# Performance work log

Measured on AMD Instinct MI355X. Metric: run time of the kernel, lower is better.

The kernel has to match this reference:

```python
import jax, jax.numpy as jnp
import numpy as np

ROPE_BASE = 10000.0
NEG_INF = jnp.finfo(jnp.float32).min


def _rope(x, pos):
    # x: [B, L, H, D], pos: [L] absolute positions. Rotate-half RoPE.
    D = x.shape[-1]
    half = D // 2
    inv_freq = 1.0 / (ROPE_BASE ** (jnp.arange(half, dtype=jnp.float32) / half))
    ang = pos.astype(jnp.float32)[:, None] * inv_freq  # [L, half]
    cos = jnp.cos(ang)[None, :, None, :]
    sin = jnp.sin(ang)[None, :, None, :]
    x1, x2 = x[..., :half], x[..., half:]
    return jnp.concatenate([x1 * cos - x2 * sin, x1 * sin + x2 * cos], axis=-1)


def setup_inputs() -> dict:
    key = jax.random.key(0)
    kq, kk, kv = jax.random.split(key, 3)
    B, L, H, Dh = 4, 4096, 16, 64
    return {
        "q": jax.random.normal(kq, (B, L, H, Dh), dtype=jnp.float32),
        "k": jax.random.normal(kk, (B, L, H, Dh), dtype=jnp.float32),
        "v": jax.random.normal(kv, (B, L, H, Dh), dtype=jnp.float32),
        "chunk_size": 1024,
        "start_index": 0,
    }


def reference(q, k, v, chunk_size, start_index):
    B, L, H, Dh = q.shape
    Dv = v.shape[-1]
    C = chunk_size
    assert L % C == 0  # chosen shapes avoid padding; original pads otherwise
    n = L // C
    # Per-chunk RoPE with offset start_index + chunk_offset equals
    # full-sequence RoPE at absolute positions start_index + arange(L).
    pos = start_index + jnp.arange(L)
    q_rot = _rope(q.astype(jnp.float32), pos)
    k_rot = _rope(k.astype(jnp.float32), pos)
    qc = q_rot.reshape(B, n, C, H, Dh)
    kc = k_rot.reshape(B, n, C, H, Dh)
    vc = v.astype(jnp.float32).reshape(B, n, C, H, Dv)
    # Unscaled (scale=1.0) block-diagonal causal attention.
    scores = jnp.einsum("bnqhd,bnkhd->bnhqk", qc, kc)
    causal = jnp.tril(jnp.ones((C, C), dtype=jnp.bool_))
    scores = jnp.where(causal, scores, NEG_INF)
    attn = jax.nn.softmax(scores, axis=-1)
    attn = jnp.where(jnp.isnan(attn), 0.0, attn)
    out = jnp.einsum("bnhqk,bnkhd->bnqhd", attn, vc)
    return out.reshape(B, L, H, Dv).astype(q.dtype)
```

## Files before the change

### kernel.cpp

```cpp
#include <hip/hip_runtime.h>

typedef _Float16 f16x8 __attribute__((ext_vector_type(8)));
typedef _Float16 f16x4 __attribute__((ext_vector_type(4)));
typedef float    f32x4 __attribute__((ext_vector_type(4)));
typedef float    f32x16 __attribute__((ext_vector_type(16)));

#define B_N    4
#define L_TOT  4096
#define H_N    16
#define DH     64
#define HALF_D 32
#define QT     64
#define KT     64
#define LDSP   72

#define LOG2_BASE 13.287712379549449f
#define LOG2E     1.4426950408889634f

#define TAB_BYTES  ((size_t)L_TOT * 64 * sizeof(float))
#define IMG_BYTES  ((size_t)B_N * H_N * 64 * 8192)

__global__ void rope_table_kernel(const int* __restrict__ sidx, float* __restrict__ tab) {
    int idx = blockIdx.x * 256 + (int)threadIdx.x;
    if (idx >= L_TOT * HALF_D) return;
    int l = idx >> 5;
    int j = idx & 31;
    float invf = exp2f(-(float)j * (LOG2_BASE / (float)HALF_D));
    float ang = (float)(sidx[0] + l) * invf;
    float s, c;
    sincosf(ang, &s, &c);
    tab[l * 64 + j] = c;
    tab[l * 64 + HALF_D + j] = s;
}

__global__ __launch_bounds__(256)
void prep_kernel(const float* __restrict__ k, const float* __restrict__ v,
                 const float* __restrict__ tab,
                 unsigned char* __restrict__ kimg, unsigned char* __restrict__ vimg)
{
    __shared__ float Vs[64][65];
    int bid = (int)blockIdx.x;
    int t = (int)threadIdx.x;

    if (bid < 4096) {
        int task = bid * 256 + t;
        int c = task & 3;
        int rowid = task >> 2;
        int l = rowid & (L_TOT - 1);
        int bh = rowid >> 12;
        int b = bh >> 4, h = bh & 15;
        int d0 = c * 8;
        const float* src = k + (((size_t)b * L_TOT + l) * H_N + h) * (size_t)DH;
        f32x4 x1a = *(const f32x4*)(src + d0);
        f32x4 x1b = *(const f32x4*)(src + d0 + 4);
        f32x4 x2a = *(const f32x4*)(src + d0 + HALF_D);
        f32x4 x2b = *(const f32x4*)(src + d0 + HALF_D + 4);
        const float* tr = tab + (size_t)l * 64 + d0;
        f32x4 ca = *(const f32x4*)(tr);
        f32x4 cb = *(const f32x4*)(tr + 4);
        f32x4 sa = *(const f32x4*)(tr + HALF_D);
        f32x4 sb = *(const f32x4*)(tr + HALF_D + 4);
        f16x8 olo, ohi;
#pragma unroll
        for (int j = 0; j < 4; ++j) {
            olo[j]     = (_Float16)(x1a[j] * ca[j] - x2a[j] * sa[j]);
            olo[j + 4] = (_Float16)(x1b[j] * cb[j] - x2b[j] * sb[j]);
            ohi[j]     = (_Float16)(x1a[j] * sa[j] + x2a[j] * ca[j]);
            ohi[j + 4] = (_Float16)(x1b[j] * sb[j] + x2b[j] * cb[j]);
        }
        size_t tile = (size_t)bh * 64 + (l >> 6);
        unsigned char* dst = kimg + tile * 8192 + (size_t)(l & 63) * 128;
        int sw = (c ^ (l & 7)) << 4;
        *(f16x8*)(dst + sw)        = olo;
        *(f16x8*)(dst + (sw ^ 64)) = ohi;
    } else {
        int vb = bid - 4096;
        int tile = vb & 63;
        int h = (vb >> 6) & 15;
        int b = vb >> 10;
        int kbase = tile * 64;
        int row = t >> 2, cb = t & 3;
        const float* src = v + (((size_t)b * L_TOT + kbase + row) * H_N + h) * (size_t)DH + cb * 16;
        f32x4 a0 = *(const f32x4*)(src);
        f32x4 a1 = *(const f32x4*)(src + 4);
        f32x4 a2 = *(const f32x4*)(src + 8);
        f32x4 a3 = *(const f32x4*)(src + 12);
#pragma unroll
        for (int j = 0; j < 4; ++j) {
            Vs[row][cb * 16 + j]      = a0[j];
            Vs[row][cb * 16 + 4 + j]  = a1[j];
            Vs[row][cb * 16 + 8 + j]  = a2[j];
            Vs[row][cb * 16 + 12 + j] = a3[j];
        }
        __syncthreads();
        size_t tbase = ((size_t)(b * 16 + h) * 64 + tile) * 8192;
#pragma unroll
        for (int e = 0; e < 2; ++e) {
            int task = e * 256 + t;
            int dv = task >> 3, c = task & 7;
            f16x8 o;
#pragma unroll
            for (int j = 0; j < 8; ++j) o[j] = (_Float16)Vs[8 * c + j][dv];
            *(f16x8*)(vimg + tbase + (size_t)dv * 128 + ((c ^ (dv & 7)) << 4)) = o;
        }
    }
}

__device__ __forceinline__ void gl_lds16(const void* g, void* lds) {
    __builtin_amdgcn_global_load_lds(
        (const __attribute__((address_space(1))) unsigned int*)g,
        (__attribute__((address_space(3))) unsigned int*)lds, 16, 0, 0);
}

__device__ __forceinline__ unsigned pku(float a, float b) {
    return __builtin_bit_cast(unsigned, __builtin_amdgcn_cvt_pkrtz(a, b));
}

__global__ __launch_bounds__(128, 2)
void attn_main_kernel(const float* __restrict__ q, const int* __restrict__ csz,
                      const float* __restrict__ tab,
                      const unsigned char* __restrict__ kimg,
                      const unsigned char* __restrict__ vimg,
                      float* __restrict__ out) {
    __shared__ __align__(16) unsigned char smem[32768];

    const int tid  = (int)threadIdx.x;
    const int lane = tid & 63;
    const int w    = tid >> 6;
    const int qi   = lane & 31;
    const int h    = lane >> 5;
    const int e7   = lane & 7;

    const int bid0  = (int)blockIdx.x;
    const int wg    = (bid0 & 7) * 512 + (bid0 >> 3);
    const int qx    = wg & 63;
    const int hh    = (wg >> 6) & 15;
    const int b     = wg >> 10;

    const int C   = csz[0];
    const int tpc = C >> 6;
    const int qtile = qx ^ ((tpc - 1) & 63);
    const int kb0 = (qtile / tpc) * tpc;

    const int qg = qtile * QT + 32 * w + qi;
    const int qloc = 32 * w + qi;

    const float* qs = q + (((size_t)b * L_TOT + qg) * H_N + hh) * (size_t)DH;
    const int d0 = 8 * h;
    f32x4 xa0 = *(const f32x4*)(qs + d0);       f32x4 xa1 = *(const f32x4*)(qs + d0 + 4);
    f32x4 xb0 = *(const f32x4*)(qs + d0 + 16);  f32x4 xb1 = *(const f32x4*)(qs + d0 + 20);
    f32x4 xc0 = *(const f32x4*)(qs + d0 + 32);  f32x4 xc1 = *(const f32x4*)(qs + d0 + 36);
    f32x4 xd0 = *(const f32x4*)(qs + d0 + 48);  f32x4 xd1 = *(const f32x4*)(qs + d0 + 52);
    const float* tr = tab + (size_t)qg * 64;
    f32x4 ca0 = *(const f32x4*)(tr + d0);       f32x4 ca1 = *(const f32x4*)(tr + d0 + 4);
    f32x4 cb0 = *(const f32x4*)(tr + d0 + 16);  f32x4 cb1 = *(const f32x4*)(tr + d0 + 20);
    f32x4 sa0 = *(const f32x4*)(tr + 32 + d0);      f32x4 sa1 = *(const f32x4*)(tr + 32 + d0 + 4);
    f32x4 sb0 = *(const f32x4*)(tr + 32 + d0 + 16); f32x4 sb1 = *(const f32x4*)(tr + 32 + d0 + 20);
    f16x8 qf0, qf1, qf2, qf3;
#pragma unroll
    for (int j = 0; j < 4; ++j) {
        qf0[j]     = (_Float16)((xa0[j] * ca0[j] - xc0[j] * sa0[j]) * LOG2E);
        qf0[j + 4] = (_Float16)((xa1[j] * ca1[j] - xc1[j] * sa1[j]) * LOG2E);
        qf1[j]     = (_Float16)((xb0[j] * cb0[j] - xd0[j] * sb0[j]) * LOG2E);
        qf1[j + 4] = (_Float16)((xb1[j] * cb1[j] - xd1[j] * sb1[j]) * LOG2E);
        qf2[j]     = (_Float16)((xa0[j] * sa0[j] + xc0[j] * ca0[j]) * LOG2E);
        qf2[j + 4] = (_Float16)((xa1[j] * sa1[j] + xc1[j] * ca1[j]) * LOG2E);
        qf3[j]     = (_Float16)((xb0[j] * sb0[j] + xd0[j] * cb0[j]) * LOG2E);
        qf3[j + 4] = (_Float16)((xb1[j] * sb1[j] + xd1[j] * cb1[j]) * LOG2E);
    }

    const unsigned char* ksrc = kimg + (size_t)(b * 16 + hh) * 64 * 8192;
    const unsigned char* vsrc = vimg + (size_t)(b * 16 + hh) * 64 * 8192;

    const int rbase = qi * 128;

    f32x16 acc0 = {}, acc1 = {};
    float m = -3e38f, l = 0.f;

    {
        const unsigned char* gk = ksrc + (size_t)kb0 * 8192;
        const unsigned char* gv = vsrc + (size_t)kb0 * 8192;
#pragma unroll
        for (int e = 0; e < 4; ++e) {
            gl_lds16(gk + tid * 16 + e * 2048, smem + tid * 16 + e * 2048);
            gl_lds16(gv + tid * 16 + e * 2048, smem + 16384 + tid * 16 + e * 2048);
        }
    }

    int pb = 0;
    for (int kb = kb0; kb <= qtile; ++kb) {
        __syncthreads();

        const char* Kb = (const char*)(smem + pb * 8192);
        const char* Vb = (const char*)(smem + 16384 + pb * 8192);
        if (kb < qtile) {
            const unsigned char* nk = ksrc + (size_t)(kb + 1) * 8192;
            const unsigned char* nv = vsrc + (size_t)(kb + 1) * 8192;
            unsigned char* lk = smem + (pb ^ 1) * 8192;
            unsigned char* lv = smem + 16384 + (pb ^ 1) * 8192;
#pragma unroll
            for (int e = 0; e < 4; ++e) {
                gl_lds16(nk + tid * 16 + e * 2048, lk + tid * 16 + e * 2048);
                gl_lds16(nv + tid * 16 + e * 2048, lv + tid * 16 + e * 2048);
            }
        }

        f32x16 sc0 = {}, sc1 = {};
        __builtin_amdgcn_s_setprio(1);
#pragma unroll
        for (int s = 0; s < 4; ++s) {
            f16x8 kf = *(const f16x8*)(Kb + rbase + (((h + 2 * s) ^ e7) << 4));
            const f16x8 qv = (s == 0) ? qf0 : (s == 1) ? qf1 : (s == 2) ? qf2 : qf3;
            sc0 = __builtin_amdgcn_mfma_f32_32x32x16_f16(kf, qv, sc0, 0, 0, 0);
        }
#pragma unroll
        for (int s = 0; s < 4; ++s) {
            f16x8 kf = *(const f16x8*)(Kb + 4096 + rbase + (((h + 2 * s) ^ e7) << 4));
            const f16x8 qv = (s == 0) ? qf0 : (s == 1) ? qf1 : (s == 2) ? qf2 : qf3;
            sc1 = __builtin_amdgcn_mfma_f32_32x32x16_f16(kf, qv, sc1, 0, 0, 0);
        }
        __builtin_amdgcn_s_setprio(0);

        if (kb == qtile) {
#pragma unroll
            for (int r = 0; r < 16; ++r) {
                const int kl = (r & 3) + 8 * (r >> 2) + 4 * h;
                if (kl > qloc)      sc0[r] = -3e38f;
                if (kl + 32 > qloc) sc1[r] = -3e38f;
            }
        }

        float m0 = sc0[0], m1 = sc0[1], m2 = sc0[2], m3 = sc0[3];
#pragma unroll
        for (int r = 4; r < 16; r += 4) {
            m0 = fmaxf(m0, sc0[r]);     m1 = fmaxf(m1, sc0[r + 1]);
            m2 = fmaxf(m2, sc0[r + 2]); m3 = fmaxf(m3, sc0[r + 3]);
        }
#pragma unroll
        for (int r = 0; r < 16; r += 4) {
            m0 = fmaxf(m0, sc1[r]);     m1 = fmaxf(m1, sc1[r + 1]);
            m2 = fmaxf(m2, sc1[r + 2]); m3 = fmaxf(m3, sc1[r + 3]);
        }
        float mx = fmaxf(fmaxf(m0, m1), fmaxf(m2, m3));
        mx = fmaxf(mx, __shfl_xor(mx, 32));
        if (__any(mx - m > 8.0f)) {
            float mn  = fmaxf(m, mx);
            float scl = exp2f(m - mn);
            m = mn;
            l *= scl;
#pragma unroll
            for (int r = 0; r < 16; ++r) { acc0[r] *= scl; acc1[r] *= scl; }
        }
        unsigned pkA[8], pkB[8];
        float s0 = 0.f, s1 = 0.f, s2 = 0.f, s3 = 0.f;
#pragma unroll
        for (int i = 0; i < 8; ++i) {
            float a0 = exp2f(sc0[2 * i] - m);
            float a1 = exp2f(sc0[2 * i + 1] - m);
            s0 += a0; s1 += a1;
            pkA[i] = pku(a0, a1);
            float b0 = exp2f(sc1[2 * i] - m);
            float b1 = exp2f(sc1[2 * i + 1] - m);
            s2 += b0; s3 += b1;
            pkB[i] = pku(b0, b1);
        }
        float ps = (s0 + s1) + (s2 + s3);
        ps += __shfl_xor(ps, 32);
        l += ps;

        __builtin_amdgcn_s_setprio(1);
#pragma unroll
        for (int ks = 0; ks < 4; ++ks) {
            const int base = 4 * (ks & 1);
            unsigned w0, w1, w2, w3;
            if (ks < 2) {
                w0 = pkA[base];     w1 = pkA[base + 1];
                w2 = pkA[base + 2]; w3 = pkA[base + 3];
            } else {
                w0 = pkB[base];     w1 = pkB[base + 1];
                w2 = pkB[base + 2]; w3 = pkB[base + 3];
            }
            unsigned x = h ? w0 : w2;
            unsigned y = h ? w1 : w3;
            unsigned xs = (unsigned)__shfl_xor((int)x, 32);
            unsigned ys = (unsigned)__shfl_xor((int)y, 32);
            uint4 fw;
            fw.x = h ? xs : w0;
            fw.y = h ? ys : w1;
            fw.z = h ? w2 : xs;
            fw.w = h ? w3 : ys;
            f16x8 pbf = __builtin_bit_cast(f16x8, fw);
            const int voff = ((h + 2 * ks) ^ e7) << 4;
            f16x8 v0 = *(const f16x8*)(Vb + rbase + voff);
            f16x8 v1 = *(const f16x8*)(Vb + 4096 + rbase + voff);
            acc0 = __builtin_amdgcn_mfma_f32_32x32x16_f16(v0, pbf, acc0, 0, 0, 0);
            acc1 = __builtin_amdgcn_mfma_f32_32x32x16_f16(v1, pbf, acc1, 0, 0, 0);
        }
        __builtin_amdgcn_s_setprio(0);

        pb ^= 1;
    }

    float inv = 1.f / l;
    float* orow = out + (((size_t)b * L_TOT + qg) * H_N + hh) * (size_t)DH;
#pragma unroll
    for (int t = 0; t < 4; ++t) {
        f32x4 v0, v1;
#pragma unroll
        for (int u = 0; u < 4; ++u) {
            v0[u] = acc0[4 * t + u] * inv;
            v1[u] = acc1[4 * t + u] * inv;
        }
        *(f32x4*)(orow + 8 * t + 4 * h)      = v0;
        *(f32x4*)(orow + 32 + 8 * t + 4 * h) = v1;
    }
}

__device__ __forceinline__ void rope_cs_inline(float pos, int d, float* cc, float* ss) {
    float invf = exp2f(-(float)d * (LOG2_BASE / (float)HALF_D));
    float s, c;
    sincosf(pos * invf, &s, &c);
    *cc = c;
    *ss = s;
}

template<bool TAB>
__global__ __launch_bounds__(256)
void chunked_attn_kernel(const float* __restrict__ q, const float* __restrict__ k,
                         const float* __restrict__ v, const int* __restrict__ csz,
                         const int* __restrict__ sidx, const float* __restrict__ tab,
                         float* __restrict__ out)
{
    __shared__ _Float16 Ks[KT][LDSP];
    __shared__ _Float16 Vt[DH][LDSP];
    __shared__ _Float16 Ps[4][16][LDSP];

    const int tid  = (int)threadIdx.x;
    const int lane = tid & 63;
    const int w    = tid >> 6;
    const int cl   = lane & 15;
    const int g    = lane >> 4;

    const int bid   = (int)blockIdx.x;
    const int qtile = bid & (L_TOT / QT - 1);
    const int h     = (bid >> 6) & (H_N - 1);
    const int b     = bid >> 10;

    const int C   = csz[0];
    const int S0  = sidx[0];
    const int tpc = C / KT;
    const int kb0 = (qtile / tpc) * tpc;

    const int qrow = qtile * QT + w * 16 + cl;
    const size_t qoff = (((size_t)b * L_TOT + qrow) * H_N + h) * (size_t)DH;
    f32x4 x1a = *(const f32x4*)(q + qoff + 8 * g);
    f32x4 x1b = *(const f32x4*)(q + qoff + 8 * g + 4);
    f32x4 x2a = *(const f32x4*)(q + qoff + 8 * g + HALF_D);
    f32x4 x2b = *(const f32x4*)(q + qoff + 8 * g + HALF_D + 4);
    f32x4 ca, cb, sa, sb;
    if (TAB) {
        const float* tr = tab + (size_t)qrow * 64 + 8 * g;
        ca = *(const f32x4*)(tr);
        cb = *(const f32x4*)(tr + 4);
        sa = *(const f32x4*)(tr + HALF_D);
        sb = *(const f32x4*)(tr + HALF_D + 4);
    } else {
        float pos = (float)(S0 + qrow);
#pragma unroll
        for (int j = 0; j < 4; ++j) {
            float c0, s0, c1, s1;
            rope_cs_inline(pos, 8 * g + j,     &c0, &s0);
            rope_cs_inline(pos, 8 * g + 4 + j, &c1, &s1);
            ca[j] = c0; sa[j] = s0;
            cb[j] = c1; sb[j] = s1;
        }
    }
    f16x8 qa0, qa1;
#pragma unroll
    for (int j = 0; j < 4; ++j) {
        qa0[j]     = (_Float16)(x1a[j] * ca[j] - x2a[j] * sa[j]);
        qa0[j + 4] = (_Float16)(x1b[j] * cb[j] - x2b[j] * sb[j]);
        qa1[j]     = (_Float16)(x1a[j] * sa[j] + x2a[j] * ca[j]);
        qa1[j + 4] = (_Float16)(x1b[j] * sb[j] + x2b[j] * cb[j]);
    }

    f32x4 o[4] = {};
    float m_r[4], l_r[4];
#pragma unroll
    for (int r = 0; r < 4; ++r) { m_r[r] = -3e38f; l_r[r] = 0.f; }

    for (int kb = kb0; kb <= qtile; ++kb) {
        __syncthreads();
        const int kbase = kb * KT;

#pragma unroll
        for (int e = 0; e < 2; ++e) {
            int task = e * 256 + tid;
            int kk = task >> 3;
            int dg = (task & 7) * 4;
            int grow = kbase + kk;
            size_t off = (((size_t)b * L_TOT + grow) * H_N + h) * (size_t)DH;
            f32x4 x1 = *(const f32x4*)(k + off + dg);
            f32x4 x2 = *(const f32x4*)(k + off + dg + HALF_D);
            f32x4 cc, ss;
            if (TAB) {
                const float* tr2 = tab + (size_t)grow * 64 + dg;
                cc = *(const f32x4*)(tr2);
                ss = *(const f32x4*)(tr2 + HALF_D);
            } else {
                float pos = (float)(S0 + grow);
#pragma unroll
                for (int j = 0; j < 4; ++j) {
                    float c0, s0;
                    rope_cs_inline(pos, dg + j, &c0, &s0);
                    cc[j] = c0; ss[j] = s0;
                }
            }
            f16x4 o1, o2;
#pragma unroll
            for (int j = 0; j < 4; ++j) {
                o1[j] = (_Float16)(x1[j] * cc[j] - x2[j] * ss[j]);
                o2[j] = (_Float16)(x1[j] * ss[j] + x2[j] * cc[j]);
            }
            *(f16x4*)&Ks[kk][dg]          = o1;
            *(f16x4*)&Ks[kk][dg + HALF_D] = o2;
        }

#pragma unroll
        for (int e = 0; e < 4; ++e) {
            int task = e * 256 + tid;
            int kk = task >> 4;
            int dq = (task & 15) * 4;
            int grow = kbase + kk;
            size_t off = (((size_t)b * L_TOT + grow) * H_N + h) * (size_t)DH + dq;
            f32x4 x = *(const f32x4*)(v + off);
#pragma unroll
            for (int i = 0; i < 4; ++i) Vt[dq + i][kk] = (_Float16)x[i];
        }
        __syncthreads();

        f32x4 sc[4];
#pragma unroll
        for (int ct = 0; ct < 4; ++ct) {
            f16x8 kf0 = *(const f16x8*)&Ks[ct * 16 + cl][8 * g];
            f16x8 kf1 = *(const f16x8*)&Ks[ct * 16 + cl][8 * g + HALF_D];
            f32x4 z = {};
            z = __builtin_amdgcn_mfma_f32_16x16x32_f16(qa0, kf0, z, 0, 0, 0);
            sc[ct] = __builtin_amdgcn_mfma_f32_16x16x32_f16(qa1, kf1, z, 0, 0, 0);
        }

        const int rowt = w * 16 + 4 * g;
        if (kb == qtile) {
#pragma unroll
            for (int ct = 0; ct < 4; ++ct)
#pragma unroll
                for (int r = 0; r < 4; ++r)
                    if (ct * 16 + cl > rowt + r) sc[ct][r] = -3e38f;
        }

        f32x4 mt;
#pragma unroll
        for (int r = 0; r < 4; ++r)
            mt[r] = fmaxf(fmaxf(sc[0][r], sc[1][r]), fmaxf(sc[2][r], sc[3][r]));
#pragma unroll
        for (int off = 1; off < 16; off <<= 1) {
#pragma unroll
            for (int r = 0; r < 4; ++r)
                mt[r] = fmaxf(mt[r], __shfl_xor(mt[r], off));
        }
        float scale_r[4];
#pragma unroll
        for (int r = 0; r < 4; ++r) {
            float mn = fmaxf(m_r[r], mt[r]);
            scale_r[r] = __expf(m_r[r] - mn);
            m_r[r] = mn;
        }
        f32x4 psum = {};
#pragma unroll
        for (int ct = 0; ct < 4; ++ct) {
#pragma unroll
            for (int r = 0; r < 4; ++r) {
                float pz = __expf(sc[ct][r] - m_r[r]);
                sc[ct][r] = pz;
                psum[r] += pz;
            }
        }
#pragma unroll
        for (int off = 1; off < 16; off <<= 1) {
#pragma unroll
            for (int r = 0; r < 4; ++r)
                psum[r] += __shfl_xor(psum[r], off);
        }
#pragma unroll
        for (int r = 0; r < 4; ++r) l_r[r] = l_r[r] * scale_r[r] + psum[r];
#pragma unroll
        for (int ct = 0; ct < 4; ++ct)
#pragma unroll
            for (int r = 0; r < 4; ++r) o[ct][r] *= scale_r[r];

#pragma unroll
        for (int ct = 0; ct < 4; ++ct)
#pragma unroll
            for (int r = 0; r < 4; ++r)
                Ps[w][4 * g + r][ct * 16 + cl] = (_Float16)sc[ct][r];

#pragma unroll
        for (int st = 0; st < 2; ++st) {
            f16x8 pa = *(const f16x8*)&Ps[w][cl][8 * g + 32 * st];
#pragma unroll
            for (int ct = 0; ct < 4; ++ct) {
                f16x8 vb = *(const f16x8*)&Vt[ct * 16 + cl][8 * g + 32 * st];
                o[ct] = __builtin_amdgcn_mfma_f32_16x16x32_f16(pa, vb, o[ct], 0, 0, 0);
            }
        }
    }

#pragma unroll
    for (int ct = 0; ct < 4; ++ct) {
#pragma unroll
        for (int r = 0; r < 4; ++r) {
            int row = qtile * QT + w * 16 + 4 * g + r;
            float val = o[ct][r] / l_r[r];
            out[(((size_t)b * L_TOT + row) * H_N + h) * (size_t)DH + ct * 16 + cl] = val;
        }
    }
}

extern "C" void kernel_launch(void* const* d_in, const int* in_sizes, int n_in,
                              void* d_out, int out_size, void* d_ws, size_t ws_size,
                              hipStream_t stream) {
    const float* q  = (const float*)d_in[0];
    const float* k  = (const float*)d_in[1];
    const float* v  = (const float*)d_in[2];
    const int* csz  = (const int*)d_in[3];
    const int* sidx = (const int*)d_in[4];
    float* out = (float*)d_out;

    const size_t TOTAL = TAB_BYTES + 2 * IMG_BYTES;
    const int grid = B_N * H_N * (L_TOT / QT);

    if (ws_size >= TOTAL) {
        float* tab = (float*)d_ws;
        unsigned char* kimg = (unsigned char*)d_ws + TAB_BYTES;
        unsigned char* vimg = kimg + IMG_BYTES;
        rope_table_kernel<<<(L_TOT * HALF_D + 255) / 256, 256, 0, stream>>>(sidx, tab);
        prep_kernel<<<8192, 256, 0, stream>>>(k, v, tab, kimg, vimg);
        attn_main_kernel<<<grid, 128, 0, stream>>>(q, csz, tab, kimg, vimg, out);
    } else if (ws_size >= TAB_BYTES) {
        float* tab = (float*)d_ws;
        rope_table_kernel<<<(L_TOT * HALF_D + 255) / 256, 256, 0, stream>>>(sidx, tab);
        chunked_attn_kernel<true><<<grid, 256, 0, stream>>>(q, k, v, csz, sidx, tab, out);
    } else {
        chunked_attn_kernel<false><<<grid, 256, 0, stream>>>(q, k, v, csz, sidx, nullptr, out);
    }
}
```

Before: 168.0 us.

## Pack two heads per workgroup with 256 threads and shared staging

Each workgroup of the main attention kernel now handles the same query tile for two adjacent heads, using four waves (two per head) instead of two. LDS doubles to 64KB so each head keeps its own double-buffered K/V tiles, and each half of the threads stages one head's tiles. The grid is halved. This cuts per-block launch and setup overhead and gives more waves per block to hide memory latency, but the larger LDS footprint may lower the number of resident blocks per CU.

```diff
diff --git a/kernel.cpp b/kernel.cpp
--- a/kernel.cpp
+++ b/kernel.cpp
@@ -116,34 +116,37 @@
     return __builtin_bit_cast(unsigned, __builtin_amdgcn_cvt_pkrtz(a, b));
 }
 
-__global__ __launch_bounds__(128, 2)
+__global__ __launch_bounds__(256, 2)
 void attn_main_kernel(const float* __restrict__ q, const int* __restrict__ csz,
                       const float* __restrict__ tab,
                       const unsigned char* __restrict__ kimg,
                       const unsigned char* __restrict__ vimg,
                       float* __restrict__ out) {
-    __shared__ __align__(16) unsigned char smem[32768];
+    __shared__ __align__(16) unsigned char smem[65536];
 
     const int tid  = (int)threadIdx.x;
     const int lane = tid & 63;
     const int w    = tid >> 6;
+    const int pair = w >> 1;
+    const int wsub = w & 1;
     const int qi   = lane & 31;
     const int h    = lane >> 5;
     const int e7   = lane & 7;
 
     const int bid0  = (int)blockIdx.x;
-    const int wg    = (bid0 & 7) * 512 + (bid0 >> 3);
+    const int wg    = (bid0 & 7) * 256 + (bid0 >> 3);
     const int qx    = wg & 63;
-    const int hh    = (wg >> 6) & 15;
-    const int b     = wg >> 10;
+    const int hp    = (wg >> 6) & 7;
+    const int b     = wg >> 9;
 
     const int C   = csz[0];
     const int tpc = C >> 6;
     const int qtile = qx ^ ((tpc - 1) & 63);
     const int kb0 = (qtile / tpc) * tpc;
 
-    const int qg = qtile * QT + 32 * w + qi;
-    const int qloc = 32 * w + qi;
+    const int hh   = 2 * hp + pair;
+    const int qg   = qtile * QT + 32 * wsub + qi;
+    const int qloc = 32 * wsub + qi;
 
     const float* qs = q + (((size_t)b * L_TOT + qg) * H_N + hh) * (size_t)DH;
     const int d0 = 8 * h;
@@ -169,8 +172,15 @@
         qf3[j + 4] = (_Float16)((xb1[j] * sb1[j] + xd1[j] * cb1[j]) * LOG2E);
     }
 
-    const unsigned char* ksrc = kimg + (size_t)(b * 16 + hh) * 64 * 8192;
-    const unsigned char* vsrc = vimg + (size_t)(b * 16 + hh) * 64 * 8192;
+    const int sh = tid >> 7;
+    const int t2 = tid & 127;
+    const unsigned char* kst = kimg + (size_t)(b * 16 + 2 * hp + sh) * 64 * 8192;
+    const unsigned char* vst = vimg + (size_t)(b * 16 + 2 * hp + sh) * 64 * 8192;
+    unsigned char* kdstB = smem + sh * 16384;
+    unsigned char* vdstB = smem + 32768 + sh * 16384;
+
+    const char* KbB = (const char*)(smem + pair * 16384);
+    const char* VbB = (const char*)(smem + 32768 + pair * 16384);
 
     const int rbase = qi * 128;
 
@@ -178,12 +188,12 @@
     float m = -3e38f, l = 0.f;
 
     {
-        const unsigned char* gk = ksrc + (size_t)kb0 * 8192;
-        const unsigned char* gv = vsrc + (size_t)kb0 * 8192;
+        const unsigned char* gk = kst + (size_t)kb0 * 8192;
+        const unsigned char* gv = vst + (size_t)kb0 * 8192;
 #pragma unroll
         for (int e = 0; e < 4; ++e) {
-            gl_lds16(gk + tid * 16 + e * 2048, smem + tid * 16 + e * 2048);
-            gl_lds16(gv + tid * 16 + e * 2048, smem + 16384 + tid * 16 + e * 2048);
+            gl_lds16(gk + t2 * 16 + e * 2048, kdstB + t2 * 16 + e * 2048);
+            gl_lds16(gv + t2 * 16 + e * 2048, vdstB + t2 * 16 + e * 2048);
         }
     }
 
@@ -191,17 +201,17 @@
     for (int kb = kb0; kb <= qtile; ++kb) {
         __syncthreads();
 
-        const char* Kb = (const char*)(smem + pb * 8192);
-        const char* Vb = (const char*)(smem + 16384 + pb * 8192);
+        const char* Kb = KbB + pb * 8192;
+        const char* Vb = VbB + pb * 8192;
         if (kb < qtile) {
-            const unsigned char* nk = ksrc + (size_t)(kb + 1) * 8192;
-            const unsigned char* nv = vsrc + (size_t)(kb + 1) * 8192;
-            unsigned char* lk = smem + (pb ^ 1) * 8192;
-            unsigned char* lv = smem + 16384 + (pb ^ 1) * 8192;
+            const unsigned char* nk = kst + (size_t)(kb + 1) * 8192;
+            const unsigned char* nv = vst + (size_t)(kb + 1) * 8192;
+            unsigned char* lk = kdstB + (pb ^ 1) * 8192;
+            unsigned char* lv = vdstB + (pb ^ 1) * 8192;
 #pragma unroll
             for (int e = 0; e < 4; ++e) {
-                gl_lds16(nk + tid * 16 + e * 2048, lk + tid * 16 + e * 2048);
-                gl_lds16(nv + tid * 16 + e * 2048, lv + tid * 16 + e * 2048);
+                gl_lds16(nk + t2 * 16 + e * 2048, lk + t2 * 16 + e * 2048);
+                gl_lds16(nv + t2 * 16 + e * 2048, lv + t2 * 16 + e * 2048);
             }
         }
 
@@ -537,7 +547,6 @@
     float* out = (float*)d_out;
 
     const size_t TOTAL = TAB_BYTES + 2 * IMG_BYTES;
-    const int grid = B_N * H_N * (L_TOT / QT);
 
     if (ws_size >= TOTAL) {
         float* tab = (float*)d_ws;
@@ -545,12 +554,12 @@
         unsigned char* vimg = kimg + IMG_BYTES;
         rope_table_kernel<<<(L_TOT * HALF_D + 255) / 256, 256, 0, stream>>>(sidx, tab);
         prep_kernel<<<8192, 256, 0, stream>>>(k, v, tab, kimg, vimg);
-        attn_main_kernel<<<grid, 128, 0, stream>>>(q, csz, tab, kimg, vimg, out);
+        attn_main_kernel<<<B_N * (H_N / 2) * (L_TOT / QT), 256, 0, stream>>>(q, csz, tab, kimg, vimg, out);
     } else if (ws_size >= TAB_BYTES) {
         float* tab = (float*)d_ws;
         rope_table_kernel<<<(L_TOT * HALF_D + 255) / 256, 256, 0, stream>>>(sidx, tab);
-        chunked_attn_kernel<true><<<grid, 256, 0, stream>>>(q, k, v, csz, sidx, tab, out);
+        chunked_attn_kernel<true><<<B_N * H_N * (L_TOT / QT), 256, 0, stream>>>(q, k, v, csz, sidx, tab, out);
     } else {
-        chunked_attn_kernel<false><<<grid, 256, 0, stream>>>(q, k, v, csz, sidx, nullptr, out);
-    }
-}
+        chunked_attn_kernel<false><<<B_N * H_N * (L_TOT / QT), 256, 0, stream>>>(q, k, v, csz, sidx, nullptr, out);
+    }
+}
```

Result: faster. 162.2 us (-3.4%).

## Replace LDS double buffering with register-staged prefetch and raise occupancy

Applied to the files above, without the earlier changes.

The next K/V tile is now prefetched into registers with ordinary global loads instead of direct global-to-LDS loads into a second buffer. This halves shared memory to 16 KB and the launch bound asks for 4 blocks per CU instead of 2. The aim is more resident waves to hide latency. In exchange each tile now needs two barriers and an extra register-to-LDS store, and the 8 uint4 staging registers add register pressure under the tighter launch bound.

```diff
diff --git a/kernel.cpp b/kernel.cpp
--- a/kernel.cpp
+++ b/kernel.cpp
@@ -106,23 +106,17 @@
     }
 }
 
-__device__ __forceinline__ void gl_lds16(const void* g, void* lds) {
-    __builtin_amdgcn_global_load_lds(
-        (const __attribute__((address_space(1))) unsigned int*)g,
-        (__attribute__((address_space(3))) unsigned int*)lds, 16, 0, 0);
-}
-
 __device__ __forceinline__ unsigned pku(float a, float b) {
     return __builtin_bit_cast(unsigned, __builtin_amdgcn_cvt_pkrtz(a, b));
 }
 
-__global__ __launch_bounds__(128, 2)
+__global__ __launch_bounds__(128, 4)
 void attn_main_kernel(const float* __restrict__ q, const int* __restrict__ csz,
                       const float* __restrict__ tab,
                       const unsigned char* __restrict__ kimg,
                       const unsigned char* __restrict__ vimg,
                       float* __restrict__ out) {
-    __shared__ __align__(16) unsigned char smem[32768];
+    __shared__ __align__(16) unsigned char smem[16384];
 
     const int tid  = (int)threadIdx.x;
     const int lane = tid & 63;
@@ -173,35 +167,38 @@
     const unsigned char* vsrc = vimg + (size_t)(b * 16 + hh) * 64 * 8192;
 
     const int rbase = qi * 128;
+    const char* Kb = (const char*)smem;
+    const char* Vb = (const char*)(smem + 8192);
 
     f32x16 acc0 = {}, acc1 = {};
     float m = -3e38f, l = 0.f;
 
+    uint4 stg[8];
     {
         const unsigned char* gk = ksrc + (size_t)kb0 * 8192;
         const unsigned char* gv = vsrc + (size_t)kb0 * 8192;
 #pragma unroll
         for (int e = 0; e < 4; ++e) {
-            gl_lds16(gk + tid * 16 + e * 2048, smem + tid * 16 + e * 2048);
-            gl_lds16(gv + tid * 16 + e * 2048, smem + 16384 + tid * 16 + e * 2048);
-        }
-    }
-
-    int pb = 0;
+            stg[e]     = *(const uint4*)(gk + tid * 16 + e * 2048);
+            stg[e + 4] = *(const uint4*)(gv + tid * 16 + e * 2048);
+        }
+#pragma unroll
+        for (int e = 0; e < 4; ++e) {
+            *(uint4*)(smem + tid * 16 + e * 2048)        = stg[e];
+            *(uint4*)(smem + 8192 + tid * 16 + e * 2048) = stg[e + 4];
+        }
+    }
+    __syncthreads();
+
     for (int kb = kb0; kb <= qtile; ++kb) {
-        __syncthreads();
-
-        const char* Kb = (const char*)(smem + pb * 8192);
-        const char* Vb = (const char*)(smem + 16384 + pb * 8192);
-        if (kb < qtile) {
-            const unsigned char* nk = ksrc + (size_t)(kb + 1) * 8192;
-            const unsigned char* nv = vsrc + (size_t)(kb + 1) * 8192;
-            unsigned char* lk = smem + (pb ^ 1) * 8192;
-            unsigned char* lv = smem + 16384 + (pb ^ 1) * 8192;
+        const bool more = (kb < qtile);
+        if (more) {
+            const unsigned char* gk = ksrc + (size_t)(kb + 1) * 8192;
+            const unsigned char* gv = vsrc + (size_t)(kb + 1) * 8192;
 #pragma unroll
             for (int e = 0; e < 4; ++e) {
-                gl_lds16(nk + tid * 16 + e * 2048, lk + tid * 16 + e * 2048);
-                gl_lds16(nv + tid * 16 + e * 2048, lv + tid * 16 + e * 2048);
+                stg[e]     = *(const uint4*)(gk + tid * 16 + e * 2048);
+                stg[e + 4] = *(const uint4*)(gv + tid * 16 + e * 2048);
             }
         }
 
@@ -298,7 +295,15 @@
         }
         __builtin_amdgcn_s_setprio(0);
 
-        pb ^= 1;
+        __syncthreads();
+        if (more) {
+#pragma unroll
+            for (int e = 0; e < 4; ++e) {
+                *(uint4*)(smem + tid * 16 + e * 2048)        = stg[e];
+                *(uint4*)(smem + 8192 + tid * 16 + e * 2048) = stg[e + 4];
+            }
+        }
+        __syncthreads();
     }
 
     float inv = 1.f / l;
```

Result: slower. 309.4 us (+84.2%).
